# Performance work log

Measured on AMD Instinct MI355X. Metric: run time of the kernel, lower is better.

## Reference

```python
import jax, jax.numpy as jnp
import numpy as np

KEEP_PROB = 0.3
KH, KW = 3, 3
STRIDE = (1, 1)
PADDING = ((1, 1), (1, 1))
DILATION = (1, 1)


def setup_inputs() -> dict:
    key = jax.random.key(0)
    k_x, k_w, k_m, k_b = jax.random.split(key, 4)
    B, C_in, H, W = 16, 64, 112, 112
    C_out = 128
    K = C_in * KH * KW  # 576
    x = jax.random.normal(k_x, (B, C_in, H, W), dtype=jnp.float32)
    weight = jax.random.normal(k_w, (C_out, K), dtype=jnp.float32)
    # binary sparsity pattern of the COO tensor, as a float mask
    mask = (jax.random.uniform(k_m, (C_out, K)) < KEEP_PROB).astype(jnp.float32)
    bias = jax.random.normal(k_b, (C_out,), dtype=jnp.float32)
    return {"x": x, "weight": weight, "mask": mask, "bias": bias}


def reference(x, weight, mask, bias):
    # Effective sparse weight matrix [C_out, C_in*kH*kW]
    spW = weight * mask
    # im2col (F.unfold): patches -> [B, C_in*kH*kW, H_out, W_out]
    # ordering of the K axis is (c, i, j) channel-major, matching torch unfold
    patches = jax.lax.conv_general_dilated_patches(
        x,
        filter_shape=(KH, KW),
        window_strides=STRIDE,
        padding=PADDING,
        rhs_dilation=DILATION,
    )  # [B, K, H_out, W_out]
    # sparse.mm(spW, X) + fold(1x1)  ==  GEMM over the K axis
    out = jnp.einsum('ok,bkhw->bohw', spW, patches)
    out = out + bias[None, :, None, None]
    return out
```

## Files before the change

### kernel.cpp

```cpp
#include <hip/hip_runtime.h>
#include <hip/hip_bf16.h>

#define C_IN    64
#define C_OUT   128
#define HH      112
#define WW      112
#define NB      16
#define KTOT    576
#define NSTEPS  36
#define NPIX    (HH*WW)
#define PH      114
#define PPIX    (PH*PH)
#define XT_OFF  147456
#define XT_BYTES ((size_t)NB * PPIX * C_IN * 2)
#define TILE_H  16
#define TILE_W  16
#define HB_X    18
#define HB_P    324
#define A_BYTES 73728
#define B_BYTES 49152
#define TY      8
#define TX      16
#define HALO_X  18
#define HALO_P  180
#define TILES_X 7
#define NTILES  98

typedef __bf16 bf16x8 __attribute__((ext_vector_type(8)));
typedef float  f32x16 __attribute__((ext_vector_type(16)));

static __device__ __forceinline__ unsigned short f2bf(float v) {
    unsigned int u = __builtin_bit_cast(unsigned int, v);
    u = u + 0x7fffu + ((u >> 16) & 1u);
    return (unsigned short)(u >> 16);
}

__global__ __launch_bounds__(256) void pack_w_kernel(
        const float* __restrict__ weight, const float* __restrict__ mask,
        unsigned short* __restrict__ pw) {
    int t  = blockIdx.x;
    int mt = threadIdx.x >> 6;
    int l  = threadIdx.x & 63;
    int g  = l >> 5;
    int m  = mt * 32 + (l & 31);
    unsigned int words[4];
    #pragma unroll
    for (int ew = 0; ew < 4; ++ew) {
        unsigned int w2[2];
        #pragma unroll
        for (int h = 0; h < 2; ++h) {
            int e    = ew * 2 + h;
            int klog = t * 16 + g * 8 + e;
            int ij   = klog >> 6;
            int c    = klog & 63;
            int ko   = c * 9 + ij;
            w2[h] = f2bf(weight[m * KTOT + ko] * mask[m * KTOT + ko]);
        }
        words[ew] = w2[0] | (w2[1] << 16);
    }
    uint4 o4; o4.x = words[0]; o4.y = words[1]; o4.z = words[2]; o4.w = words[3];
    ((uint4*)pw)[(t * 4 + mt) * 64 + l] = o4;
}

__global__ __launch_bounds__(256) void transpose_x_kernel(
        const float* __restrict__ x, unsigned short* __restrict__ xT) {
    const int b  = blockIdx.y;
    const int pp = blockIdx.x * 256 + threadIdx.x;
    if (pp >= PPIX) return;
    const int hp = pp / PH, wp = pp - hp * PH;
    const int gh = hp - 1, gw = wp - 1;
    const bool valid = (unsigned)gh < (unsigned)HH && (unsigned)gw < (unsigned)WW;
    const float* src = x + (size_t)b * C_IN * (HH * WW) + (gh * WW + gw);
    uint4* dst = (uint4*)(xT + ((size_t)b * PPIX + pp) * C_IN);
    #pragma unroll
    for (int cb = 0; cb < 8; ++cb) {
        unsigned int w4[4];
        #pragma unroll
        for (int h = 0; h < 4; ++h) {
            float v0 = valid ? src[(size_t)(cb * 8 + h * 2    ) * (HH * WW)] : 0.0f;
            float v1 = valid ? src[(size_t)(cb * 8 + h * 2 + 1) * (HH * WW)] : 0.0f;
            w4[h] = (unsigned)f2bf(v0) | ((unsigned)f2bf(v1) << 16);
        }
        uint4 o; o.x = w4[0]; o.y = w4[1]; o.z = w4[2]; o.w = w4[3];
        dst[cb] = o;
    }
}

__global__ __launch_bounds__(512, 2) void sparse_conv_mega_kernel(
        const unsigned short* __restrict__ xT, const unsigned short* __restrict__ pw,
        const float* __restrict__ bias, float* __restrict__ out) {
    __shared__ __align__(16) unsigned char smem[A_BYTES + B_BYTES];
    unsigned char* As = smem;
    unsigned char* Bs = smem + A_BYTES;

    const int bid = (blockIdx.x & 7) * 28 + (blockIdx.x >> 3);
    const int b   = bid / 14;
    const int rem = bid % 14;
    const int mh  = rem & 1;
    const int wx  = rem >> 1;
    const int w0  = wx * TILE_W;
    const int tid = threadIdx.x;
    const int wave = tid >> 6, l = tid & 63;
    const int g = l >> 5, ln = l & 31;

    const char* xTb = (const char*)xT + (size_t)b * PPIX * (C_IN * 2);

    {
        const char* pwb = (const char*)pw;
        #pragma unroll
        for (int r = 0; r < 9; ++r) {
            int c  = r * 512 + tid;
            int t  = c >> 7;
            int mt = (c >> 6) & 1;
            int ll = c & 63;
            const char* gp = pwb + (size_t)((t * 4 + mh * 2 + mt) * 64 + ll) * 16;
            char* lp = (char*)As + r * 8192 + wave * 1024;
            __builtin_amdgcn_global_load_lds(
                (const __attribute__((address_space(1))) void*)gp,
                (__attribute__((address_space(3))) void*)lp, 16, 0, 0);
        }
    }

    const int pl = wave * 32 + ln;
    const int py = pl >> 4, px = pl & 15;

    float bv[2][16];
    #pragma unroll
    for (int mtp = 0; mtp < 2; ++mtp)
        #pragma unroll
        for (int r = 0; r < 16; ++r) {
            int mloc = (r & 3) + 8 * (r >> 2) + 4 * g;
            bv[mtp][r] = bias[mh * 64 + mtp * 32 + mloc];
        }

    const size_t outb = (size_t)b * C_OUT * NPIX;

    #pragma unroll 1
    for (int it = 0; it < 7; ++it) {
        const int h0 = it * TILE_H;

        #pragma unroll
        for (int r = 0; r < 6; ++r) {
            int chunk = r * 512 + tid;
            if (chunk > HB_P * 8 - 1) chunk = HB_P * 8 - 1;
            int p = chunk >> 3, s = chunk & 7;
            int yy = p / HB_X, xx = p - yy * HB_X;
            const char* gp = xTb + (size_t)((h0 + yy) * PH + (w0 + xx)) * (C_IN * 2)
                                 + (((s ^ p) & 7) << 4);
            char* lp = (char*)Bs + r * 8192 + wave * 1024;
            __builtin_amdgcn_global_load_lds(
                (const __attribute__((address_space(1))) void*)gp,
                (__attribute__((address_space(3))) void*)lp, 16, 0, 0);
        }
        __syncthreads();

        f32x16 acc[2];
        #pragma unroll
        for (int mtp = 0; mtp < 2; ++mtp)
            #pragma unroll
            for (int q = 0; q < 16; ++q) acc[mtp][q] = 0.0f;
        #pragma unroll
        for (int mtp = 0; mtp < 2; ++mtp)
            #pragma unroll
            for (int r = 0; r < 16; ++r) acc[mtp][r] = bv[mtp][r];

        #pragma unroll 1
        for (int ij = 0; ij < 9; ++ij) {
            const int di = ij / 3, dj = ij - di * 3;
            const int Pa = (py + di) * HB_X + (px + dj);
            #pragma unroll
            for (int cs = 0; cs < 4; ++cs) {
                const int t = ij * 4 + cs;
                bf16x8 a0 = __builtin_bit_cast(bf16x8,
                    *(const uint4*)(As + ((t * 2 + 0) * 64 + l) * 16));
                bf16x8 a1 = __builtin_bit_cast(bf16x8,
                    *(const uint4*)(As + ((t * 2 + 1) * 64 + l) * 16));
                const int jb = cs * 2 + g;
                bf16x8 bb = __builtin_bit_cast(bf16x8,
                    *(const uint4*)(Bs + Pa * (C_IN * 2) + (((jb ^ Pa) & 7) << 4)));
                acc[0] = __builtin_amdgcn_mfma_f32_32x32x16_bf16(a0, bb, acc[0], 0, 0, 0);
                acc[1] = __builtin_amdgcn_mfma_f32_32x32x16_bf16(a1, bb, acc[1], 0, 0, 0);
            }
        }

        #pragma unroll
        for (int mtp = 0; mtp < 2; ++mtp) {
            #pragma unroll
            for (int r = 0; r < 16; ++r) {
                int mloc = (r & 3) + 8 * (r >> 2) + 4 * g;
                int o = mh * 64 + mtp * 32 + mloc;
                out[outb + (size_t)o * NPIX + (h0 + py) * WW + (w0 + px)] = acc[mtp][r];
            }
        }
        __syncthreads();
    }
}

__global__ __launch_bounds__(256, 4) void sparse_conv_fb_kernel(
        const float* __restrict__ x, const unsigned short* __restrict__ pw,
        const float* __restrict__ bias, float* __restrict__ out) {
    __shared__ __align__(16) unsigned short xs[HALO_P * C_IN];

    const int bid = blockIdx.x;
    const int b   = bid / NTILES;
    const int t98 = bid % NTILES;
    const int tyi = t98 / TILES_X;
    const int txi = t98 % TILES_X;
    const int h0  = tyi * TY, w0 = txi * TX;
    const int tid = threadIdx.x;

    const float* xb = x + (size_t)b * C_IN * HH * WW;
    {
        const int p  = tid;
        const bool act = p < HALO_P;
        int yy = p / HALO_X;
        int xx = p - yy * HALO_X;
        int gh = h0 + yy - 1, gw = w0 + xx - 1;
        const bool valid = act && (unsigned)gh < (unsigned)HH && (unsigned)gw < (unsigned)WW;
        const float* bp = xb + (gh * WW + gw);
        float v[C_IN];
        #pragma unroll
        for (int c = 0; c < C_IN; ++c)
            v[c] = valid ? bp[c * (HH * WW)] : 0.0f;
        if (act) {
            char* xc = (char*)xs + p * (C_IN * 2);
            #pragma unroll
            for (int j = 0; j < 8; ++j) {
                bf16x8 bvv;
                #pragma unroll
                for (int e = 0; e < 8; ++e) bvv[e] = (__bf16)v[j * 8 + e];
                *(uint4*)(xc + (((j ^ p) & 7) << 4)) = __builtin_bit_cast(uint4, bvv);
            }
        }
    }
    __syncthreads();

    const int wave = tid >> 6, l = tid & 63;
    const int wm = wave >> 1, wn = wave & 1;
    const int g  = l >> 5,  ln = l & 31;

    int P0[2];
    #pragma unroll
    for (int ntp = 0; ntp < 2; ++ntp) {
        int pt = wn * 64 + ntp * 32 + ln;
        P0[ntp] = (pt >> 4) * HALO_X + (pt & 15);
    }

    f32x16 acc[2][2];
    #pragma unroll
    for (int i = 0; i < 2; ++i)
        #pragma unroll
        for (int jq = 0; jq < 2; ++jq)
            #pragma unroll
            for (int q = 0; q < 16; ++q) acc[i][jq][q] = 0.0f;

    const uint4* __restrict__ pwv = (const uint4*)pw;

    #pragma unroll 1
    for (int ij = 0; ij < 9; ++ij) {
        const int di = ij / 3;
        const int dj = ij - di * 3;
        const int P0a = P0[0] + di * HALO_X + dj;
        const int P1a = P0[1] + di * HALO_X + dj;
        #pragma unroll
        for (int cs = 0; cs < 4; ++cs) {
            const int t = ij * 4 + cs;
            bf16x8 a0 = __builtin_bit_cast(bf16x8, pwv[(t * 4 + wm * 2 + 0) * 64 + l]);
            bf16x8 a1 = __builtin_bit_cast(bf16x8, pwv[(t * 4 + wm * 2 + 1) * 64 + l]);
            const int jb = cs * 2 + g;
            bf16x8 b0 = __builtin_bit_cast(bf16x8,
                *(const uint4*)((const char*)xs + P0a * (C_IN * 2) + (((jb ^ P0a) & 7) << 4)));
            bf16x8 b1 = __builtin_bit_cast(bf16x8,
                *(const uint4*)((const char*)xs + P1a * (C_IN * 2) + (((jb ^ P1a) & 7) << 4)));
            acc[0][0] = __builtin_amdgcn_mfma_f32_32x32x16_bf16(a0, b0, acc[0][0], 0, 0, 0);
            acc[0][1] = __builtin_amdgcn_mfma_f32_32x32x16_bf16(a0, b1, acc[0][1], 0, 0, 0);
            acc[1][0] = __builtin_amdgcn_mfma_f32_32x32x16_bf16(a1, b0, acc[1][0], 0, 0, 0);
            acc[1][1] = __builtin_amdgcn_mfma_f32_32x32x16_bf16(a1, b1, acc[1][1], 0, 0, 0);
        }
    }

    const size_t outb = (size_t)b * C_OUT * HH * WW;
    #pragma unroll
    for (int mtp = 0; mtp < 2; ++mtp) {
        #pragma unroll
        for (int r = 0; r < 16; ++r) {
            int mloc = (r & 3) + 8 * (r >> 2) + 4 * g;
            int o = (wm * 2 + mtp) * 32 + mloc;
            float bvv = bias[o];
            #pragma unroll
            for (int ntp = 0; ntp < 2; ++ntp) {
                int p  = wn * 64 + ntp * 32 + ln;
                int gh = h0 + (p >> 4), gw = w0 + (p & 15);
                out[outb + ((size_t)o * HH + gh) * WW + gw] = acc[mtp][ntp][r] + bvv;
            }
        }
    }
}

extern "C" void kernel_launch(void* const* d_in, const int* in_sizes, int n_in,
                              void* d_out, int out_size, void* d_ws, size_t ws_size,
                              hipStream_t stream) {
    const float* x    = (const float*)d_in[0];
    const float* w    = (const float*)d_in[1];
    const float* mk   = (const float*)d_in[2];
    const float* bs   = (const float*)d_in[3];
    float* out        = (float*)d_out;
    unsigned short* pw = (unsigned short*)d_ws;

    pack_w_kernel<<<dim3(NSTEPS), dim3(256), 0, stream>>>(w, mk, pw);

    if (ws_size >= (size_t)XT_OFF + XT_BYTES) {
        unsigned short* xT = (unsigned short*)((char*)d_ws + XT_OFF);
        transpose_x_kernel<<<dim3((PPIX + 255) / 256, NB), dim3(256), 0, stream>>>(x, xT);
        sparse_conv_mega_kernel<<<dim3(224), dim3(512), 0, stream>>>(xT, pw, bs, out);
    } else {
        sparse_conv_fb_kernel<<<dim3(NB * NTILES), dim3(256), 0, stream>>>(x, pw, bs, out);
    }
}
```

Baseline: 76.48 us.

## Restructure conv into 14-row bands with double-buffered LDS staging

Replaces the 16x16 column-tile kernel with a band kernel. Each block covers 14 rows and walks 7 column tiles. The next tile's halo is staged into a second LDS buffer while MFMAs run on the current one, which is meant to hide global-load latency and remove one barrier per iteration. The grid is 256 blocks of 448 threads (7 waves, each owning 2 rows), so the grid matches the CU count better, and the 36-step MFMA loop is fully unrolled. The cost is more LDS per block (double B buffer) and occupancy limited to one block per CU.

```diff
diff --git a/kernel.cpp b/kernel.cpp
--- a/kernel.cpp
+++ b/kernel.cpp
@@ -13,12 +13,11 @@
 #define PPIX    (PH*PH)
 #define XT_OFF  147456
 #define XT_BYTES ((size_t)NB * PPIX * C_IN * 2)
-#define TILE_H  16
-#define TILE_W  16
-#define HB_X    18
-#define HB_P    324
+#define BAND_H  14
+#define BH_X    18
+#define B_RECS  288
 #define A_BYTES 73728
-#define B_BYTES 49152
+#define B_BYTES 36864
 #define TY      8
 #define TX      16
 #define HALO_X  18
@@ -34,6 +33,10 @@
     u = u + 0x7fffu + ((u >> 16) & 1u);
     return (unsigned short)(u >> 16);
 }
+
+#define GLOAD_LDS(gp, lp) __builtin_amdgcn_global_load_lds( \
+    (const __attribute__((address_space(1))) void*)(gp),    \
+    (__attribute__((address_space(3))) void*)(lp), 16, 0, 0)
 
 __global__ __launch_bounds__(256) void pack_w_kernel(
         const float* __restrict__ weight, const float* __restrict__ mask,
@@ -86,20 +89,21 @@
     }
 }
 
-__global__ __launch_bounds__(512, 2) void sparse_conv_mega_kernel(
+__global__ __launch_bounds__(448, 1) void sparse_conv_band_kernel(
         const unsigned short* __restrict__ xT, const unsigned short* __restrict__ pw,
         const float* __restrict__ bias, float* __restrict__ out) {
-    __shared__ __align__(16) unsigned char smem[A_BYTES + B_BYTES];
-    unsigned char* As = smem;
-    unsigned char* Bs = smem + A_BYTES;
-
-    const int bid = (blockIdx.x & 7) * 28 + (blockIdx.x >> 3);
-    const int b   = bid / 14;
-    const int rem = bid % 14;
-    const int mh  = rem & 1;
-    const int wx  = rem >> 1;
-    const int w0  = wx * TILE_W;
-    const int tid = threadIdx.x;
+    __shared__ __align__(16) unsigned char smem[A_BYTES + 2 * B_BYTES];
+    unsigned char* As  = smem;
+    unsigned char* Bs0 = smem + A_BYTES;
+    unsigned char* Bs1 = smem + A_BYTES + B_BYTES;
+
+    const int bid  = (blockIdx.x & 7) * 32 + (blockIdx.x >> 3);
+    const int b    = bid >> 4;
+    const int rem  = bid & 15;
+    const int mh   = rem & 1;
+    const int band = rem >> 1;
+    const int h0   = band * BAND_H;
+    const int tid  = threadIdx.x;
     const int wave = tid >> 6, l = tid & 63;
     const int g = l >> 5, ln = l & 31;
 
@@ -108,91 +112,100 @@
     {
         const char* pwb = (const char*)pw;
         #pragma unroll
-        for (int r = 0; r < 9; ++r) {
-            int c  = r * 512 + tid;
+        for (int r = 0; r < 10; ++r) {
+            int c  = r * 448 + tid;
             int t  = c >> 7;
             int mt = (c >> 6) & 1;
             int ll = c & 63;
             const char* gp = pwb + (size_t)((t * 4 + mh * 2 + mt) * 64 + ll) * 16;
-            char* lp = (char*)As + r * 8192 + wave * 1024;
-            __builtin_amdgcn_global_load_lds(
-                (const __attribute__((address_space(1))) void*)gp,
-                (__attribute__((address_space(3))) void*)lp, 16, 0, 0);
-        }
-    }
-
-    const int pl = wave * 32 + ln;
-    const int py = pl >> 4, px = pl & 15;
+            GLOAD_LDS(gp, (char*)As + r * 7168 + wave * 1024);
+        }
+        if (tid < 128) {
+            int c  = 10 * 448 + tid;
+            int t  = c >> 7;
+            int mt = (c >> 6) & 1;
+            int ll = c & 63;
+            const char* gp = pwb + (size_t)((t * 4 + mh * 2 + mt) * 64 + ll) * 16;
+            GLOAD_LDS(gp, (char*)As + 10 * 7168 + wave * 1024);
+        }
+    }
+
+    auto STAGE = [&](int it, unsigned char* dst) {
+        const int w0 = it * 16;
+        #pragma unroll
+        for (int r = 0; r < 5; ++r) {
+            int chunk = r * 448 + tid;
+            int p = chunk >> 3, s = chunk & 7;
+            int yy = p / BH_X, xx = p - yy * BH_X;
+            const char* gp = xTb + (size_t)((h0 + yy) * PH + (w0 + xx)) * (C_IN * 2)
+                                 + (((s ^ p) & 7) << 4);
+            GLOAD_LDS(gp, (char*)dst + r * 7168 + wave * 1024);
+        }
+        if (tid < 64) {
+            int chunk = 5 * 448 + tid;
+            int p = chunk >> 3, s = chunk & 7;
+            int yy = p / BH_X, xx = p - yy * BH_X;
+            const char* gp = xTb + (size_t)((h0 + yy) * PH + (w0 + xx)) * (C_IN * 2)
+                                 + (((s ^ p) & 7) << 4);
+            GLOAD_LDS(gp, (char*)dst + 5 * 7168 + wave * 1024);
+        }
+    };
+
+    const int py = 2 * wave + (ln >> 4);
+    const int px = ln & 15;
 
     float bv[2][16];
     #pragma unroll
-    for (int mtp = 0; mtp < 2; ++mtp)
+    for (int mt = 0; mt < 2; ++mt)
         #pragma unroll
         for (int r = 0; r < 16; ++r) {
             int mloc = (r & 3) + 8 * (r >> 2) + 4 * g;
-            bv[mtp][r] = bias[mh * 64 + mtp * 32 + mloc];
-        }
+            bv[mt][r] = bias[mh * 64 + mt * 32 + mloc];
+        }
+
+    STAGE(0, Bs0);
+    __syncthreads();
 
     const size_t outb = (size_t)b * C_OUT * NPIX;
 
     #pragma unroll 1
     for (int it = 0; it < 7; ++it) {
-        const int h0 = it * TILE_H;
-
-        #pragma unroll
-        for (int r = 0; r < 6; ++r) {
-            int chunk = r * 512 + tid;
-            if (chunk > HB_P * 8 - 1) chunk = HB_P * 8 - 1;
-            int p = chunk >> 3, s = chunk & 7;
-            int yy = p / HB_X, xx = p - yy * HB_X;
-            const char* gp = xTb + (size_t)((h0 + yy) * PH + (w0 + xx)) * (C_IN * 2)
-                                 + (((s ^ p) & 7) << 4);
-            char* lp = (char*)Bs + r * 8192 + wave * 1024;
-            __builtin_amdgcn_global_load_lds(
-                (const __attribute__((address_space(1))) void*)gp,
-                (__attribute__((address_space(3))) void*)lp, 16, 0, 0);
-        }
-        __syncthreads();
+        unsigned char* curB = (it & 1) ? Bs1 : Bs0;
+        unsigned char* nxtB = (it & 1) ? Bs0 : Bs1;
+        if (it < 6) STAGE(it + 1, nxtB);
 
         f32x16 acc[2];
         #pragma unroll
-        for (int mtp = 0; mtp < 2; ++mtp)
-            #pragma unroll
-            for (int q = 0; q < 16; ++q) acc[mtp][q] = 0.0f;
-        #pragma unroll
-        for (int mtp = 0; mtp < 2; ++mtp)
-            #pragma unroll
-            for (int r = 0; r < 16; ++r) acc[mtp][r] = bv[mtp][r];
-
-        #pragma unroll 1
-        for (int ij = 0; ij < 9; ++ij) {
+        for (int mt = 0; mt < 2; ++mt)
+            #pragma unroll
+            for (int r = 0; r < 16; ++r) acc[mt][r] = bv[mt][r];
+
+        #pragma unroll
+        for (int t = 0; t < NSTEPS; ++t) {
+            const int ij = t >> 2, cs = t & 3;
             const int di = ij / 3, dj = ij - di * 3;
-            const int Pa = (py + di) * HB_X + (px + dj);
-            #pragma unroll
-            for (int cs = 0; cs < 4; ++cs) {
-                const int t = ij * 4 + cs;
-                bf16x8 a0 = __builtin_bit_cast(bf16x8,
-                    *(const uint4*)(As + ((t * 2 + 0) * 64 + l) * 16));
-                bf16x8 a1 = __builtin_bit_cast(bf16x8,
-                    *(const uint4*)(As + ((t * 2 + 1) * 64 + l) * 16));
-                const int jb = cs * 2 + g;
-                bf16x8 bb = __builtin_bit_cast(bf16x8,
-                    *(const uint4*)(Bs + Pa * (C_IN * 2) + (((jb ^ Pa) & 7) << 4)));
-                acc[0] = __builtin_amdgcn_mfma_f32_32x32x16_bf16(a0, bb, acc[0], 0, 0, 0);
-                acc[1] = __builtin_amdgcn_mfma_f32_32x32x16_bf16(a1, bb, acc[1], 0, 0, 0);
-            }
-        }
-
-        #pragma unroll
-        for (int mtp = 0; mtp < 2; ++mtp) {
+            const int jb = cs * 2 + g;
+            bf16x8 a0 = __builtin_bit_cast(bf16x8,
+                *(const uint4*)(As + ((t * 2 + 0) * 64 + l) * 16));
+            bf16x8 a1 = __builtin_bit_cast(bf16x8,
+                *(const uint4*)(As + ((t * 2 + 1) * 64 + l) * 16));
+            const int Pa = (py + di) * BH_X + (px + dj);
+            bf16x8 bb = __builtin_bit_cast(bf16x8,
+                *(const uint4*)(curB + Pa * 128 + (((jb ^ Pa) & 7) << 4)));
+            acc[0] = __builtin_amdgcn_mfma_f32_32x32x16_bf16(a0, bb, acc[0], 0, 0, 0);
+            acc[1] = __builtin_amdgcn_mfma_f32_32x32x16_bf16(a1, bb, acc[1], 0, 0, 0);
+        }
+
+        #pragma unroll
+        for (int mt = 0; mt < 2; ++mt)
             #pragma unroll
             for (int r = 0; r < 16; ++r) {
                 int mloc = (r & 3) + 8 * (r >> 2) + 4 * g;
-                int o = mh * 64 + mtp * 32 + mloc;
-                out[outb + (size_t)o * NPIX + (h0 + py) * WW + (w0 + px)] = acc[mtp][r];
+                int o = mh * 64 + mt * 32 + mloc;
+                out[outb + (size_t)o * NPIX + (h0 + py) * WW + it * 16 + px] = acc[mt][r];
             }
-        }
-        __syncthreads();
+
+        if (it < 6) __syncthreads();
     }
 }
 
@@ -312,7 +325,7 @@
     if (ws_size >= (size_t)XT_OFF + XT_BYTES) {
         unsigned short* xT = (unsigned short*)((char*)d_ws + XT_OFF);
         transpose_x_kernel<<<dim3((PPIX + 255) / 256, NB), dim3(256), 0, stream>>>(x, xT);
-        sparse_conv_mega_kernel<<<dim3(224), dim3(512), 0, stream>>>(xT, pw, bs, out);
+        sparse_conv_band_kernel<<<dim3(256), dim3(448), 0, stream>>>(xT, pw, bs, out);
     } else {
         sparse_conv_fb_kernel<<<dim3(NB * NTILES), dim3(256), 0, stream>>>(x, pw, bs, out);
     }
```

After: 72.24 us. 1.06x faster.
